# Kernel tuning notes

Measured on AMD Instinct MI355X. Metric: run time of the kernel, lower is better.

## Reference

```python
import jax, jax.numpy as jnp
import numpy as np

NUM_CLIPS = 64
# (kernel, stride) per layer for each scale, per num_scale_layers=[16,8,8]
SCALE_SPECS = [[(1, 1)] + [(2, 1)] * 15,
               [(3, 2)] + [(2, 1)] * 7,
               [(3, 2)] + [(2, 1)] * 7]
KEEP = {0: (7, 15), 1: (3, 7), 2: (3, 5, 7)}


def _build_props():
    # replicates SparsePropMaxPool.__init__ construction of self.props
    tmp = [[1] * 16, [2] + [1] * 7, [2] + [1] * 7]
    acum, stride, props = 0, 1, []
    for scale_idx, strides in enumerate(tmp):
        for i, st in enumerate(strides):
            stride *= st
            if i in KEEP[scale_idx]:
                s = np.arange(0, NUM_CLIPS - acum - i * stride, stride)
                props.append(np.stack([s, s + acum + i * stride], -1))
        acum += stride * (len(strides) + 1)
    props = np.concatenate(props, 0)
    props[:, 1] += 1
    return props.astype(np.int64)  # [153, 2]


def _maxpool1d(x, k, s):
    if k == 1 and s == 1:
        return x
    return jax.lax.reduce_window(x, -jnp.inf, jax.lax.max,
                                 (1, 1, k), (1, 1, s), 'VALID')


def _forward(x, props):
    B, H, N = x.shape  # N == 64
    acum, stride = 0, 1
    s_parts, e_parts, feat_parts = [], [], []
    for scale in SCALE_SPECS:
        for i, (k, st) in enumerate(scale):
            stride *= st
            x = _maxpool1d(x, k, st)
            s = np.arange(0, N - acum - i * stride, stride)
            s_parts.append(s)
            e_parts.append(s + acum + i * stride)
            feat_parts.append(x)  # [B, H, len(s)]
        acum += stride * (len(scale) + 1)
    # all (s,e) diagonals are disjoint across layers -> one fused scatter
    s_all = np.concatenate(s_parts)
    e_all = np.concatenate(e_parts)
    feats = jnp.concatenate(feat_parts, axis=-1)  # [B, H, total]
    ori_map_h = jnp.zeros((B, H, N, N), x.dtype).at[:, :, s_all, e_all].set(feats)
    ori_map_mask = jnp.zeros((B, 1, N, N), x.dtype).at[:, :, s_all, e_all].set(1.0)
    p0, p1 = props[:, 0], props[:, 1] - 1
    props_h = jnp.transpose(ori_map_h[:, :, p0, p1], (0, 2, 1))  # [B, P, H]
    # faithful (no-op) write-back as in the torch source
    ori_map_h = ori_map_h.at[:, :, p0, p1].set(jnp.transpose(props_h, (0, 2, 1)))
    return props_h, ori_map_h, ori_map_mask


def setup_inputs() -> dict:
    key = jax.random.key(0)
    kx, kg = jax.random.split(key)
    x = jax.random.normal(kx, (64, 512, 64), dtype=jnp.float32)
    props = jnp.asarray(_build_props())  # [153, 2]
    props_graph = jax.random.randint(kg, (153, 153), 0, 2, dtype=jnp.int32)
    return {'x': x, 'props': props, 'props_graph': props_graph}


def reference(x, props, props_graph):
    return _forward(x, props)
```

## Files before the change

kernel.cpp:

```cpp
#include <hip/hip_runtime.h>


#define B_ 64
#define H_ 512
#define N_ 64
#define NPROP 153

typedef float f4 __attribute__((ext_vector_type(4)));

__device__ __forceinline__ bool in_set(int s, int d) {
    if (d < 0) return false;
    if (d <= 15) return true;
    if (d <= 31) return (d & 1) && ((s & 1) == 0);
    return (d >= 35) && ((d & 3) == 3) && ((s & 3) == 0);
}

__global__ __launch_bounds__(256) void fused_kernel(const float* __restrict__ x,
                                                    float* __restrict__ out_props,
                                                    float* __restrict__ out_map,
                                                    float* __restrict__ out_mask) {
    const int tid = threadIdx.x;
    const int bid = blockIdx.x;

    __shared__ __align__(16) float xs[16][72];

    if (bid < B_) {
        const int b = bid;

        f4* mk = reinterpret_cast<f4*>(out_mask + (size_t)b * (N_ * N_));
        #pragma unroll
        for (int i = 0; i < 4; ++i) {
            const int idx = tid + 256 * i;
            const int s = idx >> 4, c = idx & 15;
            f4 w;
            w.x = in_set(s, 4 * c + 0 - s) ? 1.f : 0.f;
            w.y = in_set(s, 4 * c + 1 - s) ? 1.f : 0.f;
            w.z = in_set(s, 4 * c + 2 - s) ? 1.f : 0.f;
            w.w = in_set(s, 4 * c + 3 - s) ? 1.f : 0.f;
            __builtin_nontemporal_store(w, &mk[idx]);
        }

        #pragma unroll 1
        for (int half = 0; half < 2; ++half) {
            const int h = tid + 256 * half;
            const f4* xr = reinterpret_cast<const f4*>(x + ((size_t)b * H_ + h) * N_);
            float r[64];
            #pragma unroll
            for (int k = 0; k < 16; ++k) {
                f4 v = xr[k];
                r[4*k+0] = v.x; r[4*k+1] = v.y; r[4*k+2] = v.z; r[4*k+3] = v.w;
            }
            float a[63];
            #pragma unroll
            for (int i = 0; i < 63; ++i) a[i] = fmaxf(r[i], r[i+1]);
            float m4[61];
            #pragma unroll
            for (int i = 0; i < 61; ++i) m4[i] = fmaxf(a[i], a[i+2]);
            float T3[57];
            #pragma unroll
            for (int i = 0; i < 57; ++i) T3[i] = fmaxf(m4[i], m4[i+4]);

            float* po = out_props + (size_t)b * NPROP * H_ + h;
            int p = 0;
            #pragma unroll
            for (int s = 0; s < 57; ++s)
                __builtin_nontemporal_store(T3[s], &po[(size_t)(p++) * H_]);
            #pragma unroll
            for (int s = 0; s < 49; ++s)
                __builtin_nontemporal_store(fmaxf(T3[s], T3[s + 8]),
                                            &po[(size_t)(p++) * H_]);
            #pragma unroll
            for (int s = 0; s <= 40; s += 2)
                __builtin_nontemporal_store(fmaxf(fmaxf(T3[s], T3[s + 8]), T3[s + 16]),
                                            &po[(size_t)(p++) * H_]);
            #pragma unroll
            for (int s = 0; s <= 32; s += 2)
                __builtin_nontemporal_store(
                    fmaxf(fmaxf(T3[s], T3[s + 8]), fmaxf(T3[s + 16], T3[s + 24])),
                    &po[(size_t)(p++) * H_]);
            #pragma unroll
            for (int s = 0; s <= 16; s += 4) {
                float m = T3[s];
                #pragma unroll
                for (int j = 8; j <= 40; j += 8) m = fmaxf(m, T3[s + j]);
                __builtin_nontemporal_store(m, &po[(size_t)(p++) * H_]);
            }
            #pragma unroll
            for (int s = 0; s <= 8; s += 4) {
                float m = T3[s];
                #pragma unroll
                for (int j = 8; j <= 48; j += 8) m = fmaxf(m, T3[s + j]);
                __builtin_nontemporal_store(m, &po[(size_t)(p++) * H_]);
            }
            {
                float m = T3[0];
                #pragma unroll
                for (int j = 8; j <= 56; j += 8) m = fmaxf(m, T3[j]);
                __builtin_nontemporal_store(m, &po[(size_t)p * H_]);
            }
        }
        return;
    }

    const int mb = bid - B_;
    const int g  = tid >> 4;
    const int t  = tid & 15;
    const size_t bh = (size_t)mb * 16 + g;

    f4 xv = reinterpret_cast<const f4*>(x)[mb * 256 + tid];
    *reinterpret_cast<f4*>(&xs[g][4 * t]) = xv;
    __syncthreads();

    f4* mrow = reinterpret_cast<f4*>(out_map + bh * (size_t)(N_ * N_));
    const int e0 = 4 * t;
    float vx = 0.f, vy = 0.f, vz = 0.f, vw = 0.f;
    #pragma unroll
    for (int s = N_ - 1; s >= 0; --s) {
        const float mv = xs[g][s];
        vx = (s == e0 + 0) ? mv : fmaxf(vx, mv);
        vy = (s == e0 + 1) ? mv : fmaxf(vy, mv);
        vz = (s == e0 + 2) ? mv : fmaxf(vz, mv);
        vw = (s == e0 + 3) ? mv : fmaxf(vw, mv);
        f4 w;
        w.x = in_set(s, e0 + 0 - s) ? vx : 0.f;
        w.y = in_set(s, e0 + 1 - s) ? vy : 0.f;
        w.z = in_set(s, e0 + 2 - s) ? vz : 0.f;
        w.w = in_set(s, e0 + 3 - s) ? vw : 0.f;
        mrow[s * 16 + t] = w;
    }
}

extern "C" void kernel_launch(void* const* d_in, const int* in_sizes, int n_in,
                              void* d_out, int out_size, void* d_ws, size_t ws_size,
                              hipStream_t stream) {
    const float* x = (const float*)d_in[0];
    float* out       = (float*)d_out;
    float* out_props = out;
    float* out_map   = out + (size_t)B_ * NPROP * H_;
    float* out_mask  = out_map + (size_t)B_ * H_ * N_ * N_;

    fused_kernel<<<dim3(B_ + B_ * H_ / 16), dim3(256), 0, stream>>>(
        x, out_props, out_map, out_mask);
}
```

Before: 104.8 us.

## Restructure map writer to one wave per row with shuffle-based window maxes

The map-writing blocks now give each 64-lane wave a single (b,h) row, instead of 16 threads per row. Sliding-window maxima of widths 1–4 are built with wave shuffles and kept in shared memory. Each lane walks s in steps of 4 and keeps a running max per column, so every store instruction writes one contiguous 1KB span with nontemporal hints. This is meant to improve write coalescing and cache behaviour on the store-bound output, at the cost of four times as many blocks. It relies on wave-lockstep shared-memory visibility, since there is no barrier.

```diff
diff --git a/kernel.cpp b/kernel.cpp
--- a/kernel.cpp
+++ b/kernel.cpp
@@ -21,8 +21,6 @@
                                                     float* __restrict__ out_mask) {
     const int tid = threadIdx.x;
     const int bid = blockIdx.x;
-
-    __shared__ __align__(16) float xs[16][72];
 
     if (bid < B_) {
         const int b = bid;
@@ -103,30 +101,42 @@
     }
 
     const int mb = bid - B_;
-    const int g  = tid >> 4;
-    const int t  = tid & 15;
-    const size_t bh = (size_t)mb * 16 + g;
+    const int w  = tid >> 6;
+    const int l  = tid & 63;
+    const size_t bh = (size_t)mb * 4 + w;
 
-    f4 xv = reinterpret_cast<const f4*>(x)[mb * 256 + tid];
-    *reinterpret_cast<f4*>(&xs[g][4 * t]) = xv;
-    __syncthreads();
+    __shared__ float W[4][4][68];
 
-    f4* mrow = reinterpret_cast<f4*>(out_map + bh * (size_t)(N_ * N_));
-    const int e0 = 4 * t;
-    float vx = 0.f, vy = 0.f, vz = 0.f, vw = 0.f;
+    const float xv = x[bh * N_ + l];
+    const float x1 = __shfl_down(xv, 1);
+    const float w1 = fmaxf(xv, x1);
+    const float x2 = __shfl_down(xv, 2);
+    const float w2 = fmaxf(w1, x2);
+    const float w12 = __shfl_down(w1, 2);
+    const float w3 = fmaxf(w1, w12);
+    W[w][0][l] = xv; W[w][1][l] = w1; W[w][2][l] = w2; W[w][3][l] = w3;
+
+    const int j = l >> 4;
+    const int t = l & 15;
+    float* orow = out_map + bh * (size_t)(N_ * N_) + (size_t)l * 4;
+
+    float vrun[4] = {0.f, 0.f, 0.f, 0.f};
     #pragma unroll
-    for (int s = N_ - 1; s >= 0; --s) {
-        const float mv = xs[g][s];
-        vx = (s == e0 + 0) ? mv : fmaxf(vx, mv);
-        vy = (s == e0 + 1) ? mv : fmaxf(vy, mv);
-        vz = (s == e0 + 2) ? mv : fmaxf(vz, mv);
-        vw = (s == e0 + 3) ? mv : fmaxf(vw, mv);
-        f4 w;
-        w.x = in_set(s, e0 + 0 - s) ? vx : 0.f;
-        w.y = in_set(s, e0 + 1 - s) ? vy : 0.f;
-        w.z = in_set(s, e0 + 2 - s) ? vz : 0.f;
-        w.w = in_set(s, e0 + 3 - s) ? vw : 0.f;
-        mrow[s * 16 + t] = w;
+    for (int sb = 15; sb >= 0; --sb) {
+        const int s = 4 * sb + j;
+        float oo[4];
+        #pragma unroll
+        for (int c = 0; c < 4; ++c) {
+            const int e = 4 * t + c;
+            const int d = e - s;
+            const int rr = d < 0 ? 0 : (d > 3 ? 3 : d);
+            const float tv = W[w][rr][s];
+            const float nv = (d <= 3) ? tv : fmaxf(vrun[c], tv);
+            vrun[c] = nv;
+            oo[c] = in_set(s, d) ? nv : 0.f;
+        }
+        f4 o = {oo[0], oo[1], oo[2], oo[3]};
+        __builtin_nontemporal_store(o, reinterpret_cast<f4*>(orow + sb * 256));
     }
 }
 
@@ -139,6 +149,6 @@
     float* out_map   = out + (size_t)B_ * NPROP * H_;
     float* out_mask  = out_map + (size_t)B_ * H_ * N_ * N_;
 
-    fused_kernel<<<dim3(B_ + B_ * H_ / 16), dim3(256), 0, stream>>>(
+    fused_kernel<<<dim3(B_ + B_ * H_ / 4), dim3(256), 0, stream>>>(
         x, out_props, out_map, out_mask);
 }
```

New measurement: 109.4 us. 4.4% more time.
